# Performance work log

Measured on AMD Instinct MI355X. Metric: run time of the kernel, lower is better.

Reference implementation:

```python
import jax, jax.numpy as jnp
import numpy as np

DT = 0.01
T, B, I, H, O = 512, 128, 256, 1024, 256


def setup_inputs() -> dict:
    key = jax.random.key(0)
    ks = jax.random.split(key, 9)
    def xavier(k, out_f, in_f):
        lim = np.sqrt(6.0 / (in_f + out_f)).astype(np.float32)
        return jax.random.uniform(k, (out_f, in_f), jnp.float32, -lim, lim)
    return {
        "x": jax.random.normal(ks[0], (T, B, I), jnp.float32),
        "W_h": xavier(ks[1], H, I + H),                      # HRCell linear, no bias
        "gain": jnp.ones((H,), jnp.float32),
        "omega": jax.random.uniform(ks[2], (H,), jnp.float32, 10.0, 50.0),
        "b_offset": jax.random.uniform(ks[3], (H,), jnp.float32, 1.0, 6.0),
        "W_o": xavier(ks[4], H, H),                          # LICell linear, no bias
        "tau_mem": 20.0 + 5.0 * jax.random.normal(ks[5], (H,), jnp.float32),
        "W_out": xavier(ks[6], O, H),                        # readout Linear
        "b_out": jnp.zeros((O,), jnp.float32),
    }


def reference(x, W_h, gain, omega, b_offset, W_o, tau_mem, W_out, b_out):
    om = jnp.abs(omega)
    om2 = om * om
    b = om2 * 0.005 + jnp.abs(b_offset)          # damping coefficient per unit
    alpha = jnp.exp(-1.0 / jnp.abs(tau_mem))     # leaky-integrator decay
    Bsz = x.shape[1]
    Hd = W_h.shape[0]
    Od = W_out.shape[0]

    def step(carry, x_t):
        hu, hv, ou, acc = carry
        # HRCell: linear on concat(input, hidden_u), then harmonic update
        in_sum = jnp.concatenate([x_t, hu], axis=1) @ W_h.T   # [B, H]
        hv = hv + hu * DT
        hu = hu + in_sum * DT - b * hu * (2.0 * DT) - om2 * hv * DT
        hu = hu * gain                                        # normalize=False path
        # LICell: leaky integrator on projected hidden
        ou = ou * alpha + (hu @ W_o.T) * (1.0 - alpha)
        # readout, summed over time
        acc = acc + ou @ W_out.T + b_out
        return (hu, hv, ou, acc), None

    z = jnp.zeros((Bsz, Hd), x.dtype)
    init = (z, z, z, jnp.zeros((Bsz, Od), x.dtype))
    (hu, hv, ou, acc), _ = jax.lax.scan(step, init, x)
    return acc
```

## Files before the change

kernel.cpp:

```cpp
#include <hip/hip_runtime.h>
#include <math.h>

#define DT 0.01f
constexpr int T = 512, B = 128, I = 256, H = 1024, O = 256;
constexpr int K = I + H;

constexpr size_t OFF_OSUM  = 0;
constexpr size_t OFF_HUH0  = OFF_OSUM + (size_t)B * H;
constexpr size_t OFF_HUL0  = OFF_HUH0 + (size_t)B * H / 2;
constexpr size_t OFF_HUH1  = OFF_HUL0 + (size_t)B * H / 2;
constexpr size_t OFF_HUL1  = OFF_HUH1 + (size_t)B * H / 2;
constexpr size_t OFF_COEF  = OFF_HUL1 + (size_t)B * H / 2;
constexpr size_t OFF_FLAGS = OFF_COEF + 5 * (size_t)H;
constexpr size_t OFF_WHH   = OFF_FLAGS + 8192;
constexpr size_t OFF_WHL   = OFF_WHH + 64 * 40 * 64 * 8 / 2;
constexpr size_t OFF_WOH   = OFF_WHL + 64 * 40 * 64 * 8 / 2;
constexpr size_t OFF_WOL   = OFF_WOH + 64 * 32 * 64 * 8 / 2;

constexpr int SM_WHH  = 0;
constexpr int SM_WHL  = 65536;
constexpr int SM_REDS = 131072;
constexpr int SM_REDP = 139520;
constexpr int SM_BYTES = 147968;

typedef __attribute__((ext_vector_type(8))) short short8v;
typedef __attribute__((ext_vector_type(4))) float f32x4;

static __device__ inline short f2bf(float f) {
    unsigned u = __builtin_bit_cast(unsigned, f);
    u += 0x7fffu + ((u >> 16) & 1u);
    return (short)(u >> 16);
}
static __device__ inline float bf2f(short s) {
    return __builtin_bit_cast(float, ((unsigned)(unsigned short)s) << 16);
}

__global__ __launch_bounds__(256)
void init_kernel(float* __restrict__ ws, const float* __restrict__ omega,
                 const float* __restrict__ b_offset, const float* __restrict__ tau_mem,
                 const float* __restrict__ gain) {
    size_t tid = (size_t)blockIdx.x * blockDim.x + threadIdx.x;
    size_t stride = (size_t)gridDim.x * blockDim.x;
    for (size_t i = tid; i < (size_t)B * H; i += stride) ws[OFF_HUH0 + i] = 0.0f;
    for (size_t i = tid; i < 8192; i += stride) ws[OFF_FLAGS + i] = 0.0f;
    if (tid < H) {
        float om  = fabsf(omega[tid]);
        float om2 = om * om;
        float bb  = om2 * 0.005f + fabsf(b_offset[tid]);
        float al  = expf(-1.0f / fabsf(tau_mem[tid]));
        float g   = gain[tid];
        ws[OFF_COEF + 0 * H + tid] = g * (1.0f - 2.0f * bb * DT);
        ws[OFF_COEF + 1 * H + tid] = g * DT;
        ws[OFF_COEF + 2 * H + tid] = g * om2 * DT;
        ws[OFF_COEF + 3 * H + tid] = al;
        ws[OFF_COEF + 4 * H + tid] = 1.0f - al;
    }
}

template <int NKS, int KD>
__global__ __launch_bounds__(256)
void convert_kernel(const float* __restrict__ W, short* __restrict__ WH,
                    short* __restrict__ WL) {
    int g = blockIdx.x * 256 + threadIdx.x;
    int lane = g & 63;
    int ks = (g >> 6) % NKS;
    int cg = g / (NKS * 64);
    int col = cg * 16 + (lane & 15);
    int k = ks * 32 + ((lane >> 4) << 3);
    const float* src = W + (size_t)col * KD + k;
    short8v hi, lo;
    #pragma unroll
    for (int j = 0; j < 8; ++j) {
        float v = src[j];
        short h = f2bf(v);
        hi[j] = h;
        lo[j] = f2bf(v - bf2f(h));
    }
    *(short8v*)(WH + (size_t)g * 8) = hi;
    *(short8v*)(WL + (size_t)g * 8) = lo;
}

__global__ __launch_bounds__(512)
void rnn_persist(const float* __restrict__ x, float* __restrict__ ws) {
    extern __shared__ char sm[];
    float* redS = (float*)(sm + SM_REDS);
    float* redP = (float*)(sm + SM_REDP);
    __shared__ int role_sm;

    const float* coef = ws + OFF_COEF;
    float* osum_g = ws + OFF_OSUM;
    const short* huhS[2] = {(const short*)(ws + OFF_HUH0), (const short*)(ws + OFF_HUH1)};
    const short* hulS[2] = {(const short*)(ws + OFF_HUL0), (const short*)(ws + OFF_HUL1)};
    unsigned int* huhW[2] = {(unsigned int*)(ws + OFF_HUH0), (unsigned int*)(ws + OFF_HUH1)};
    unsigned int* hulW[2] = {(unsigned int*)(ws + OFF_HUL0), (unsigned int*)(ws + OFF_HUL1)};
    int* flags = (int*)(ws + OFF_FLAGS);
    int* ctr   = flags + 4096;

    const int tid = threadIdx.x;

    if (tid == 0) {
        unsigned xcc_;
        asm volatile("s_getreg_b32 %0, hwreg(HW_REG_XCC_ID)" : "=s"(xcc_));
        int slot = atomicAdd(ctr + (xcc_ & 7), 1);
        role_sm = (int)((xcc_ & 7) * 32 + (slot & 31));
    }
    __syncthreads();
    const int role = role_sm;
    const int xcc = role >> 5;
    const int g   = role & 31;
    const int col0 = g * 32, row0 = xcc * 16;

    const int wid = tid >> 6, lane = tid & 63;
    const int ntile = wid & 1, ksl = wid >> 1;
    const int colgrp = 2 * g + ntile;
    const int rowg = row0 + (lane & 15);
    const int koff = (lane >> 4) << 3;

    {
        const float4* srcH = (const float4*)(ws + OFF_WHH);
        const float4* srcL = (const float4*)(ws + OFF_WHL);
        float4* dH = (float4*)(sm + SM_WHH);
        float4* dL = (float4*)(sm + SM_WHL);
        for (int i = tid; i < 2 * 2048; i += 512) {
            int n = i >> 11, rem = i & 2047;
            dH[i] = srcH[((size_t)(2 * g + n) * 40 + 8) * 64 + rem];
            dL[i] = srcL[((size_t)(2 * g + n) * 40 + 8) * 64 + rem];
        }
    }
    short8v woh[8], wxh[2], wxl[2];
    {
        const short8v* WOHg = (const short8v*)(ws + OFF_WOH) + (size_t)colgrp * 32 * 64 + lane;
        const short8v* WXH  = (const short8v*)(ws + OFF_WHH) + (size_t)colgrp * 40 * 64 + lane;
        const short8v* WXL  = (const short8v*)(ws + OFF_WHL) + (size_t)colgrp * 40 * 64 + lane;
        #pragma unroll
        for (int j = 0; j < 8; ++j) woh[j] = WOHg[(ksl * 8 + j) * 64];
        #pragma unroll
        for (int j = 0; j < 2; ++j) { wxh[j] = WXH[(ksl * 2 + j) * 64]; wxl[j] = WXL[(ksl * 2 + j) * 64]; }
    }
    __syncthreads();

    const short8v* lWHH = (const short8v*)(sm + SM_WHH) + (size_t)ntile * 2048 + lane;
    const short8v* lWHL = (const short8v*)(sm + SM_WHL) + (size_t)ntile * 2048 + lane;

    const int er = tid >> 4;
    const int ec0 = (tid & 15) * 2;
    const int gcol0 = col0 + ec0;
    const size_t erow = (size_t)(row0 + (er & 15));
    float k1a=0,k1b=0,k2a=0,k2b=0,k3a=0,k3b=0, ala=0,alb=0,alma=0,almb=0;
    if (tid < 256) {
        k1a = coef[gcol0];         k1b = coef[gcol0 + 1];
        k2a = coef[H + gcol0];     k2b = coef[H + gcol0 + 1];
        k3a = coef[2 * H + gcol0]; k3b = coef[2 * H + gcol0 + 1];
        ala = coef[3 * H + gcol0]; alb = coef[3 * H + gcol0 + 1];
        alma = coef[4 * H + gcol0]; almb = coef[4 * H + gcol0 + 1];
    }
    float hva=0,hvb=0,oua=0,oub=0,osa=0,osb=0,hua=0,hub=0;

    int* myflag = flags + ((xcc * 32 + g) << 4);
    const size_t rowOffH = (size_t)rowg * H + koff;

    for (int s = 0; s <= T; ++s) {
        const bool last = (s == T);
        f32x4 accS = {0, 0, 0, 0}, accP = {0, 0, 0, 0};

        if (!last) {
            const float* xrow = x + (size_t)s * B * I + (size_t)rowg * I + koff;
            #pragma unroll
            for (int j = 0; j < 2; ++j) {
                float4 a0 = *(const float4*)(xrow + (ksl * 2 + j) * 32);
                float4 a1 = *(const float4*)(xrow + (ksl * 2 + j) * 32 + 4);
                float av[8] = {a0.x,a0.y,a0.z,a0.w,a1.x,a1.y,a1.z,a1.w};
                short8v ah, alv;
                #pragma unroll
                for (int q = 0; q < 8; ++q) {
                    short h = f2bf(av[q]);
                    ah[q] = h;
                    alv[q] = f2bf(av[q] - bf2f(h));
                }
                accS = __builtin_amdgcn_mfma_f32_16x16x32_bf16(ah, wxh[j], accS, 0,0,0);
                accS = __builtin_amdgcn_mfma_f32_16x16x32_bf16(alv, wxh[j], accS, 0,0,0);
                accS = __builtin_amdgcn_mfma_f32_16x16x32_bf16(ah, wxl[j], accS, 0,0,0);
            }
        }

        if (tid < 32) {
            int* pollp = flags + ((xcc * 32 + tid) << 4);
            while (__hip_atomic_load(pollp, __ATOMIC_RELAXED, __HIP_MEMORY_SCOPE_AGENT) < s)
                __builtin_amdgcn_s_sleep(1);
        }
        __syncthreads();
        asm volatile("" ::: "memory");

        const short* hb_ = huhS[s & 1] + rowOffH;
        const short* lb_ = hulS[s & 1] + rowOffH;
        short8v hbuf[8], lbuf[8];
        #pragma unroll
        for (int j = 0; j < 8; ++j) {
            asm volatile("global_load_dwordx4 %0, %1, off sc0" : "=v"(hbuf[j]) : "v"(hb_ + (ksl * 8 + j) * 32));
            asm volatile("global_load_dwordx4 %0, %1, off sc0" : "=v"(lbuf[j]) : "v"(lb_ + (ksl * 8 + j) * 32));
        }
        if (s > 0 && tid < 256) {
            const float* rp = redP + er * 33 + ec0;
            float p0 = (rp[0] + rp[528]) + (rp[1056] + rp[1584]);
            float p1 = (rp[1] + rp[529]) + (rp[1057] + rp[1585]);
            oua = oua * ala + p0 * alma; osa += oua;
            oub = oub * alb + p1 * almb; osb += oub;
        }

        if (!last) {
            asm volatile("s_waitcnt vmcnt(8)");
            __builtin_amdgcn_sched_barrier(0);
            #pragma unroll
            for (int j = 0; j < 4; ++j) {
                short8v ch = lWHH[(ksl * 8 + j) * 64];
                short8v cl = lWHL[(ksl * 8 + j) * 64];
                accS = __builtin_amdgcn_mfma_f32_16x16x32_bf16(hbuf[j], ch, accS, 0,0,0);
                accS = __builtin_amdgcn_mfma_f32_16x16x32_bf16(lbuf[j], ch, accS, 0,0,0);
                accS = __builtin_amdgcn_mfma_f32_16x16x32_bf16(hbuf[j], cl, accS, 0,0,0);
            }
            asm volatile("s_waitcnt vmcnt(0)");
            __builtin_amdgcn_sched_barrier(0);
            #pragma unroll
            for (int j = 4; j < 8; ++j) {
                short8v ch = lWHH[(ksl * 8 + j) * 64];
                short8v cl = lWHL[(ksl * 8 + j) * 64];
                accS = __builtin_amdgcn_mfma_f32_16x16x32_bf16(hbuf[j], ch, accS, 0,0,0);
                accS = __builtin_amdgcn_mfma_f32_16x16x32_bf16(lbuf[j], ch, accS, 0,0,0);
                accS = __builtin_amdgcn_mfma_f32_16x16x32_bf16(hbuf[j], cl, accS, 0,0,0);
            }
            #pragma unroll
            for (int r = 0; r < 4; ++r) {
                int crow = ((lane >> 4) << 2) + r;
                redS[ksl * 528 + crow * 33 + ntile * 16 + (lane & 15)] = accS[r];
            }
            __syncthreads();

            if (tid < 256) {
                const float* rs = redS + er * 33 + ec0;
                float s0 = (rs[0] + rs[528]) + (rs[1056] + rs[1584]);
                float s1 = (rs[1] + rs[529]) + (rs[1057] + rs[1585]);
                float hvn0 = hva + hua * DT;
                float hun0 = k1a * hua + k2a * s0 - k3a * hvn0;
                hva = hvn0; hua = hun0;
                float hvn1 = hvb + hub * DT;
                float hun1 = k1b * hub + k2b * s1 - k3b * hvn1;
                hvb = hvn1; hub = hun1;
                short h0 = f2bf(hun0), h1 = f2bf(hun1);
                short l0 = f2bf(hun0 - bf2f(h0)), l1 = f2bf(hun1 - bf2f(h1));
                unsigned hp = (unsigned)(unsigned short)h0 | ((unsigned)(unsigned short)h1 << 16);
                unsigned lp = (unsigned)(unsigned short)l0 | ((unsigned)(unsigned short)l1 << 16);
                size_t off32 = (erow * H + gcol0) >> 1;
                unsigned int* hp_ = huhW[(s + 1) & 1] + off32;
                unsigned int* lp_ = hulW[(s + 1) & 1] + off32;
                asm volatile("global_store_dword %0, %1, off sc0" :: "v"(hp_), "v"(hp) : "memory");
                asm volatile("global_store_dword %0, %1, off sc0" :: "v"(lp_), "v"(lp) : "memory");
            }
            asm volatile("s_waitcnt vmcnt(0)" ::: "memory");
            __syncthreads();
            if (tid == 0)
                __hip_atomic_store(myflag, s + 1, __ATOMIC_RELAXED, __HIP_MEMORY_SCOPE_AGENT);
        } else {
            asm volatile("s_waitcnt vmcnt(0)");
            __builtin_amdgcn_sched_barrier(0);
            __syncthreads();
        }

        #pragma unroll
        for (int j = 0; j < 8; ++j) {
            accP = __builtin_amdgcn_mfma_f32_16x16x32_bf16(hbuf[j], woh[j], accP, 0,0,0);
            accP = __builtin_amdgcn_mfma_f32_16x16x32_bf16(lbuf[j], woh[j], accP, 0,0,0);
        }
        #pragma unroll
        for (int r = 0; r < 4; ++r) {
            int crow = ((lane >> 4) << 2) + r;
            redP[ksl * 528 + crow * 33 + ntile * 16 + (lane & 15)] = accP[r];
        }
    }

    __syncthreads();
    if (tid < 256) {
        const float* rp = redP + er * 33 + ec0;
        float p0 = (rp[0] + rp[528]) + (rp[1056] + rp[1584]);
        float p1 = (rp[1] + rp[529]) + (rp[1057] + rp[1585]);
        float o0 = oua * ala + p0 * alma; osa += o0;
        float o1 = oub * alb + p1 * almb; osb += o1;
        osum_g[erow * H + gcol0] = osa;
        osum_g[erow * H + gcol0 + 1] = osb;
    }
}

__global__ __launch_bounds__(256)
void readout_kernel(const float* __restrict__ ou_sum, const float* __restrict__ W_out,
                    const float* __restrict__ b_out, float* __restrict__ out) {
    constexpr int KC = 128, BT = 32, CT = 16;
    __shared__ float act[BT][KC + 4];
    __shared__ float w[CT][KC + 4];
    int wg = blockIdx.x;
    int bt = wg & 3, cg = wg >> 2;
    int row0 = bt * BT, col0 = cg * CT;
    int tid = threadIdx.x;
    int c = tid & 15, rr = tid >> 4;

    float4 acc0 = {0, 0, 0, 0}, acc1 = {0, 0, 0, 0};
    for (int kc = 0; kc < H / KC; ++kc) {
        int k0 = kc * KC;
        for (int i = tid; i < BT * (KC / 4); i += 256) {
            int r = i >> 5, c4 = (i & 31) * 4;
            *(float4*)&act[r][c4] = *(const float4*)&ou_sum[(size_t)(row0 + r) * H + k0 + c4];
        }
        for (int i = tid; i < CT * (KC / 4); i += 256) {
            int r = i >> 5, c4 = (i & 31) * 4;
            *(float4*)&w[r][c4] = *(const float4*)&W_out[(size_t)(col0 + r) * H + k0 + c4];
        }
        __syncthreads();
        #pragma unroll
        for (int k4 = 0; k4 < KC / 4; ++k4) {
            float4 a0 = *(const float4*)&act[rr][k4 * 4];
            float4 a1 = *(const float4*)&act[rr + 16][k4 * 4];
            float4 w0 = *(const float4*)&w[c][k4 * 4];
            acc0.x = fmaf(a0.x, w0.x, acc0.x); acc0.y = fmaf(a0.y, w0.y, acc0.y);
            acc0.z = fmaf(a0.z, w0.z, acc0.z); acc0.w = fmaf(a0.w, w0.w, acc0.w);
            acc1.x = fmaf(a1.x, w0.x, acc1.x); acc1.y = fmaf(a1.y, w0.y, acc1.y);
            acc1.z = fmaf(a1.z, w0.z, acc1.z); acc1.w = fmaf(a1.w, w0.w, acc1.w);
        }
        __syncthreads();
    }
    float v0 = (acc0.x + acc0.y) + (acc0.z + acc0.w);
    float v1 = (acc1.x + acc1.y) + (acc1.z + acc1.w);
    int gcol = col0 + c;
    float bo = b_out[gcol] * (float)T;
    out[(size_t)(row0 + rr) * O + gcol] = v0 + bo;
    out[(size_t)(row0 + rr + 16) * O + gcol] = v1 + bo;
}

extern "C" void kernel_launch(void* const* d_in, const int* in_sizes, int n_in,
                              void* d_out, int out_size, void* d_ws, size_t ws_size,
                              hipStream_t stream) {
    const float* x        = (const float*)d_in[0];
    const float* W_h      = (const float*)d_in[1];
    const float* gain     = (const float*)d_in[2];
    const float* omega    = (const float*)d_in[3];
    const float* b_offset = (const float*)d_in[4];
    const float* W_o      = (const float*)d_in[5];
    const float* tau_mem  = (const float*)d_in[6];
    const float* W_out    = (const float*)d_in[7];
    const float* b_out    = (const float*)d_in[8];
    float* ws  = (float*)d_ws;
    float* out = (float*)d_out;

    init_kernel<<<512, 256, 0, stream>>>(ws, omega, b_offset, tau_mem, gain);
    convert_kernel<40, K><<<640, 256, 0, stream>>>(
        W_h, (short*)(ws + OFF_WHH), (short*)(ws + OFF_WHL));
    convert_kernel<32, H><<<512, 256, 0, stream>>>(
        W_o, (short*)(ws + OFF_WOH), (short*)(ws + OFF_WOL));

    rnn_persist<<<256, 512, SM_BYTES, stream>>>(x, ws);

    readout_kernel<<<64, 256, 0, stream>>>(ws + OFF_OSUM, W_out, b_out, out);
}
```

Measured before the change: 3.717 ms.

## Split MFMA accumulators and add fast sc0 flag polling with safe fallback

Each MFMA reduction chain now alternates between two accumulators, which shortens the dependency chain between back-to-back MFMAs. Inter-block step flags are duplicated: a fast copy is written and polled with sc0 plain loads/stores, and a safe copy uses agent-scope atomics and is checked every 64 spins. The aim is lower latency in the per-step cross-workgroup barrier of the persistent recurrent kernel. The fast flag path relies on cache coherence behaviour that is not guaranteed, so the atomic fallback is there to avoid hangs.

```diff
diff --git a/kernel.cpp b/kernel.cpp
--- a/kernel.cpp
+++ b/kernel.cpp
@@ -12,7 +12,7 @@
 constexpr size_t OFF_HUL1  = OFF_HUH1 + (size_t)B * H / 2;
 constexpr size_t OFF_COEF  = OFF_HUL1 + (size_t)B * H / 2;
 constexpr size_t OFF_FLAGS = OFF_COEF + 5 * (size_t)H;
-constexpr size_t OFF_WHH   = OFF_FLAGS + 8192;
+constexpr size_t OFF_WHH   = OFF_FLAGS + 8256;
 constexpr size_t OFF_WHL   = OFF_WHH + 64 * 40 * 64 * 8 / 2;
 constexpr size_t OFF_WOH   = OFF_WHL + 64 * 40 * 64 * 8 / 2;
 constexpr size_t OFF_WOL   = OFF_WOH + 64 * 32 * 64 * 8 / 2;
@@ -42,7 +42,7 @@
     size_t tid = (size_t)blockIdx.x * blockDim.x + threadIdx.x;
     size_t stride = (size_t)gridDim.x * blockDim.x;
     for (size_t i = tid; i < (size_t)B * H; i += stride) ws[OFF_HUH0 + i] = 0.0f;
-    for (size_t i = tid; i < 8192; i += stride) ws[OFF_FLAGS + i] = 0.0f;
+    for (size_t i = tid; i < 8256; i += stride) ws[OFF_FLAGS + i] = 0.0f;
     if (tid < H) {
         float om  = fabsf(omega[tid]);
         float om2 = om * om;
@@ -94,7 +94,7 @@
     unsigned int* huhW[2] = {(unsigned int*)(ws + OFF_HUH0), (unsigned int*)(ws + OFF_HUH1)};
     unsigned int* hulW[2] = {(unsigned int*)(ws + OFF_HUL0), (unsigned int*)(ws + OFF_HUL1)};
     int* flags = (int*)(ws + OFF_FLAGS);
-    int* ctr   = flags + 4096;
+    int* ctr   = flags + 8192;
 
     const int tid = threadIdx.x;
 
@@ -156,12 +156,16 @@
     }
     float hva=0,hvb=0,oua=0,oub=0,osa=0,osb=0,hua=0,hub=0;
 
-    int* myflag = flags + ((xcc * 32 + g) << 4);
+    int* myfast = flags + ((xcc * 32 + g) << 4);
+    int* mysafe = flags + 4096 + ((xcc * 32 + g) << 4);
+    const int* fastp = flags + ((xcc * 32 + (tid & 31)) << 4);
+    int* safep = flags + 4096 + ((xcc * 32 + (tid & 31)) << 4);
     const size_t rowOffH = (size_t)rowg * H + koff;
 
     for (int s = 0; s <= T; ++s) {
         const bool last = (s == T);
-        f32x4 accS = {0, 0, 0, 0}, accP = {0, 0, 0, 0};
+        f32x4 accS = {0,0,0,0}, accS2 = {0,0,0,0};
+        f32x4 accP = {0,0,0,0}, accP2 = {0,0,0,0};
 
         if (!last) {
             const float* xrow = x + (size_t)s * B * I + (size_t)rowg * I + koff;
@@ -177,16 +181,25 @@
                     ah[q] = h;
                     alv[q] = f2bf(av[q] - bf2f(h));
                 }
-                accS = __builtin_amdgcn_mfma_f32_16x16x32_bf16(ah, wxh[j], accS, 0,0,0);
-                accS = __builtin_amdgcn_mfma_f32_16x16x32_bf16(alv, wxh[j], accS, 0,0,0);
-                accS = __builtin_amdgcn_mfma_f32_16x16x32_bf16(ah, wxl[j], accS, 0,0,0);
+                f32x4* acc = j ? &accS2 : &accS;
+                *acc = __builtin_amdgcn_mfma_f32_16x16x32_bf16(ah, wxh[j], *acc, 0,0,0);
+                *acc = __builtin_amdgcn_mfma_f32_16x16x32_bf16(alv, wxh[j], *acc, 0,0,0);
+                *acc = __builtin_amdgcn_mfma_f32_16x16x32_bf16(ah, wxl[j], *acc, 0,0,0);
             }
         }
 
         if (tid < 32) {
-            int* pollp = flags + ((xcc * 32 + tid) << 4);
-            while (__hip_atomic_load(pollp, __ATOMIC_RELAXED, __HIP_MEMORY_SCOPE_AGENT) < s)
+            int v, spins = 0;
+            for (;;) {
+                asm volatile("global_load_dword %0, %1, off sc0\n\ts_waitcnt vmcnt(0)"
+                             : "=v"(v) : "v"(fastp) : "memory");
+                if (v >= s) break;
+                if ((++spins & 63) == 0) {
+                    v = __hip_atomic_load(safep, __ATOMIC_RELAXED, __HIP_MEMORY_SCOPE_AGENT);
+                    if (v >= s) break;
+                }
                 __builtin_amdgcn_s_sleep(1);
+            }
         }
         __syncthreads();
         asm volatile("" ::: "memory");
@@ -214,9 +227,10 @@
             for (int j = 0; j < 4; ++j) {
                 short8v ch = lWHH[(ksl * 8 + j) * 64];
                 short8v cl = lWHL[(ksl * 8 + j) * 64];
-                accS = __builtin_amdgcn_mfma_f32_16x16x32_bf16(hbuf[j], ch, accS, 0,0,0);
-                accS = __builtin_amdgcn_mfma_f32_16x16x32_bf16(lbuf[j], ch, accS, 0,0,0);
-                accS = __builtin_amdgcn_mfma_f32_16x16x32_bf16(hbuf[j], cl, accS, 0,0,0);
+                f32x4* acc = (j & 1) ? &accS2 : &accS;
+                *acc = __builtin_amdgcn_mfma_f32_16x16x32_bf16(hbuf[j], ch, *acc, 0,0,0);
+                *acc = __builtin_amdgcn_mfma_f32_16x16x32_bf16(lbuf[j], ch, *acc, 0,0,0);
+                *acc = __builtin_amdgcn_mfma_f32_16x16x32_bf16(hbuf[j], cl, *acc, 0,0,0);
             }
             asm volatile("s_waitcnt vmcnt(0)");
             __builtin_amdgcn_sched_barrier(0);
@@ -224,14 +238,15 @@
             for (int j = 4; j < 8; ++j) {
                 short8v ch = lWHH[(ksl * 8 + j) * 64];
                 short8v cl = lWHL[(ksl * 8 + j) * 64];
-                accS = __builtin_amdgcn_mfma_f32_16x16x32_bf16(hbuf[j], ch, accS, 0,0,0);
-                accS = __builtin_amdgcn_mfma_f32_16x16x32_bf16(lbuf[j], ch, accS, 0,0,0);
-                accS = __builtin_amdgcn_mfma_f32_16x16x32_bf16(hbuf[j], cl, accS, 0,0,0);
+                f32x4* acc = (j & 1) ? &accS2 : &accS;
+                *acc = __builtin_amdgcn_mfma_f32_16x16x32_bf16(hbuf[j], ch, *acc, 0,0,0);
+                *acc = __builtin_amdgcn_mfma_f32_16x16x32_bf16(lbuf[j], ch, *acc, 0,0,0);
+                *acc = __builtin_amdgcn_mfma_f32_16x16x32_bf16(hbuf[j], cl, *acc, 0,0,0);
             }
             #pragma unroll
             for (int r = 0; r < 4; ++r) {
                 int crow = ((lane >> 4) << 2) + r;
-                redS[ksl * 528 + crow * 33 + ntile * 16 + (lane & 15)] = accS[r];
+                redS[ksl * 528 + crow * 33 + ntile * 16 + (lane & 15)] = accS[r] + accS2[r];
             }
             __syncthreads();
 
@@ -257,8 +272,11 @@
             }
             asm volatile("s_waitcnt vmcnt(0)" ::: "memory");
             __syncthreads();
-            if (tid == 0)
-                __hip_atomic_store(myflag, s + 1, __ATOMIC_RELAXED, __HIP_MEMORY_SCOPE_AGENT);
+            if (tid == 0) {
+                int fv = s + 1;
+                asm volatile("global_store_dword %0, %1, off sc0" :: "v"(myfast), "v"(fv) : "memory");
+                __hip_atomic_store(mysafe, fv, __ATOMIC_RELAXED, __HIP_MEMORY_SCOPE_AGENT);
+            }
         } else {
             asm volatile("s_waitcnt vmcnt(0)");
             __builtin_amdgcn_sched_barrier(0);
@@ -267,13 +285,14 @@
 
         #pragma unroll
         for (int j = 0; j < 8; ++j) {
-            accP = __builtin_amdgcn_mfma_f32_16x16x32_bf16(hbuf[j], woh[j], accP, 0,0,0);
-            accP = __builtin_amdgcn_mfma_f32_16x16x32_bf16(lbuf[j], woh[j], accP, 0,0,0);
+            f32x4* acc = (j & 1) ? &accP2 : &accP;
+            *acc = __builtin_amdgcn_mfma_f32_16x16x32_bf16(hbuf[j], woh[j], *acc, 0,0,0);
+            *acc = __builtin_amdgcn_mfma_f32_16x16x32_bf16(lbuf[j], woh[j], *acc, 0,0,0);
         }
         #pragma unroll
         for (int r = 0; r < 4; ++r) {
             int crow = ((lane >> 4) << 2) + r;
-            redP[ksl * 528 + crow * 33 + ntile * 16 + (lane & 15)] = accP[r];
+            redP[ksl * 528 + crow * 33 + ntile * 16 + (lane & 15)] = accP[r] + accP2[r];
         }
     }
 
```

After: 3.790 ms. No clear change (+2.0%).

## Split persistent workgroups into recurrence and output-projection roles with reader flags

Applied to the files above, without the earlier changes.

The persistent RNN kernel now splits each XCC's 32 workgroups into two roles. Sixteen compute the hidden recurrence over 64-column tiles. The other sixteen compute the W_o projection and leaky integration from the published hidden state, one step behind. Recurrence workgroups now wait on both writer and reader flags before overwriting the double buffer. The goal is to take the W_o matmul off the serial critical path of the recurrence. The cost is that each recurrence workgroup does twice the K-columns, streams W_h low-part weights from global memory every step, and carries extra cross-workgroup synchronization.

```diff
diff --git a/kernel.cpp b/kernel.cpp
--- a/kernel.cpp
+++ b/kernel.cpp
@@ -12,16 +12,13 @@
 constexpr size_t OFF_HUL1  = OFF_HUH1 + (size_t)B * H / 2;
 constexpr size_t OFF_COEF  = OFF_HUL1 + (size_t)B * H / 2;
 constexpr size_t OFF_FLAGS = OFF_COEF + 5 * (size_t)H;
-constexpr size_t OFF_WHH   = OFF_FLAGS + 8192;
+constexpr size_t OFF_WHH   = OFF_FLAGS + 8224;
 constexpr size_t OFF_WHL   = OFF_WHH + 64 * 40 * 64 * 8 / 2;
 constexpr size_t OFF_WOH   = OFF_WHL + 64 * 40 * 64 * 8 / 2;
 constexpr size_t OFF_WOL   = OFF_WOH + 64 * 32 * 64 * 8 / 2;
 
-constexpr int SM_WHH  = 0;
-constexpr int SM_WHL  = 65536;
-constexpr int SM_REDS = 131072;
-constexpr int SM_REDP = 139520;
-constexpr int SM_BYTES = 147968;
+constexpr int SM_RED   = 131072;
+constexpr int SM_BYTES = 131072 + 2 * 16 * 68 * 4;
 
 typedef __attribute__((ext_vector_type(8))) short short8v;
 typedef __attribute__((ext_vector_type(4))) float f32x4;
@@ -42,7 +39,7 @@
     size_t tid = (size_t)blockIdx.x * blockDim.x + threadIdx.x;
     size_t stride = (size_t)gridDim.x * blockDim.x;
     for (size_t i = tid; i < (size_t)B * H; i += stride) ws[OFF_HUH0 + i] = 0.0f;
-    for (size_t i = tid; i < 8192; i += stride) ws[OFF_FLAGS + i] = 0.0f;
+    for (size_t i = tid; i < 8224; i += stride) ws[OFF_FLAGS + i] = 0.0f;
     if (tid < H) {
         float om  = fabsf(omega[tid]);
         float om2 = om * om;
@@ -83,18 +80,17 @@
 __global__ __launch_bounds__(512)
 void rnn_persist(const float* __restrict__ x, float* __restrict__ ws) {
     extern __shared__ char sm[];
-    float* redS = (float*)(sm + SM_REDS);
-    float* redP = (float*)(sm + SM_REDP);
+    float* red = (float*)(sm + SM_RED);
     __shared__ int role_sm;
 
     const float* coef = ws + OFF_COEF;
     float* osum_g = ws + OFF_OSUM;
     const short* huhS[2] = {(const short*)(ws + OFF_HUH0), (const short*)(ws + OFF_HUH1)};
     const short* hulS[2] = {(const short*)(ws + OFF_HUL0), (const short*)(ws + OFF_HUL1)};
-    unsigned int* huhW[2] = {(unsigned int*)(ws + OFF_HUH0), (unsigned int*)(ws + OFF_HUH1)};
-    unsigned int* hulW[2] = {(unsigned int*)(ws + OFF_HUL0), (unsigned int*)(ws + OFF_HUL1)};
+    short* huhW[2] = {(short*)(ws + OFF_HUH0), (short*)(ws + OFF_HUH1)};
+    short* hulW[2] = {(short*)(ws + OFF_HUL0), (short*)(ws + OFF_HUL1)};
     int* flags = (int*)(ws + OFF_FLAGS);
-    int* ctr   = flags + 4096;
+    int* ctr   = flags + 8192;
 
     const int tid = threadIdx.x;
 
@@ -106,186 +102,244 @@
     }
     __syncthreads();
     const int role = role_sm;
-    const int xcc = role >> 5;
-    const int g   = role & 31;
-    const int col0 = g * 32, row0 = xcc * 16;
+    const int xcc  = role >> 5;
+    const int slot = role & 31;
+    const bool isZ = (slot < 16);
+    const int g    = slot & 15;
+    const int row0 = xcc * 16;
 
     const int wid = tid >> 6, lane = tid & 63;
-    const int ntile = wid & 1, ksl = wid >> 1;
-    const int colgrp = 2 * g + ntile;
+    const int cgl = wid & 3, ksl = wid >> 2;
+    const int cg16 = 4 * g + cgl;
     const int rowg = row0 + (lane & 15);
     const int koff = (lane >> 4) << 3;
-
-    {
-        const float4* srcH = (const float4*)(ws + OFF_WHH);
-        const float4* srcL = (const float4*)(ws + OFF_WHL);
-        float4* dH = (float4*)(sm + SM_WHH);
-        float4* dL = (float4*)(sm + SM_WHL);
-        for (int i = tid; i < 2 * 2048; i += 512) {
-            int n = i >> 11, rem = i & 2047;
-            dH[i] = srcH[((size_t)(2 * g + n) * 40 + 8) * 64 + rem];
-            dL[i] = srcL[((size_t)(2 * g + n) * 40 + 8) * 64 + rem];
-        }
-    }
-    short8v woh[8], wxh[2], wxl[2];
-    {
-        const short8v* WOHg = (const short8v*)(ws + OFF_WOH) + (size_t)colgrp * 32 * 64 + lane;
-        const short8v* WXH  = (const short8v*)(ws + OFF_WHH) + (size_t)colgrp * 40 * 64 + lane;
-        const short8v* WXL  = (const short8v*)(ws + OFF_WHL) + (size_t)colgrp * 40 * 64 + lane;
-        #pragma unroll
-        for (int j = 0; j < 8; ++j) woh[j] = WOHg[(ksl * 8 + j) * 64];
-        #pragma unroll
-        for (int j = 0; j < 2; ++j) { wxh[j] = WXH[(ksl * 2 + j) * 64]; wxl[j] = WXL[(ksl * 2 + j) * 64]; }
-    }
-    __syncthreads();
-
-    const short8v* lWHH = (const short8v*)(sm + SM_WHH) + (size_t)ntile * 2048 + lane;
-    const short8v* lWHL = (const short8v*)(sm + SM_WHL) + (size_t)ntile * 2048 + lane;
+    const size_t rowOff = (size_t)rowg * H + koff;
+
+    int* flagbase = flags + xcc * 1024;
+    int* mywrite  = flagbase + g * 16;
+    int* myread   = flagbase + (16 + slot) * 16;
 
     const int er = tid >> 4;
-    const int ec0 = (tid & 15) * 2;
-    const int gcol0 = col0 + ec0;
+    const int c0 = (tid & 15) * 4;
+    const int gcol0 = g * 64 + c0;
     const size_t erow = (size_t)(row0 + (er & 15));
-    float k1a=0,k1b=0,k2a=0,k2b=0,k3a=0,k3b=0, ala=0,alb=0,alma=0,almb=0;
-    if (tid < 256) {
-        k1a = coef[gcol0];         k1b = coef[gcol0 + 1];
-        k2a = coef[H + gcol0];     k2b = coef[H + gcol0 + 1];
-        k3a = coef[2 * H + gcol0]; k3b = coef[2 * H + gcol0 + 1];
-        ala = coef[3 * H + gcol0]; alb = coef[3 * H + gcol0 + 1];
-        alma = coef[4 * H + gcol0]; almb = coef[4 * H + gcol0 + 1];
-    }
-    float hva=0,hvb=0,oua=0,oub=0,osa=0,osb=0,hua=0,hub=0;
-
-    int* myflag = flags + ((xcc * 32 + g) << 4);
-    const size_t rowOffH = (size_t)rowg * H + koff;
-
-    for (int s = 0; s <= T; ++s) {
-        const bool last = (s == T);
-        f32x4 accS = {0, 0, 0, 0}, accP = {0, 0, 0, 0};
-
-        if (!last) {
-            const float* xrow = x + (size_t)s * B * I + (size_t)rowg * I + koff;
-            #pragma unroll
-            for (int j = 0; j < 2; ++j) {
-                float4 a0 = *(const float4*)(xrow + (ksl * 2 + j) * 32);
-                float4 a1 = *(const float4*)(xrow + (ksl * 2 + j) * 32 + 4);
-                float av[8] = {a0.x,a0.y,a0.z,a0.w,a1.x,a1.y,a1.z,a1.w};
-                short8v ah, alv;
-                #pragma unroll
-                for (int q = 0; q < 8; ++q) {
-                    short h = f2bf(av[q]);
-                    ah[q] = h;
-                    alv[q] = f2bf(av[q] - bf2f(h));
-                }
-                accS = __builtin_amdgcn_mfma_f32_16x16x32_bf16(ah, wxh[j], accS, 0,0,0);
-                accS = __builtin_amdgcn_mfma_f32_16x16x32_bf16(alv, wxh[j], accS, 0,0,0);
-                accS = __builtin_amdgcn_mfma_f32_16x16x32_bf16(ah, wxl[j], accS, 0,0,0);
-            }
-        }
-
-        if (tid < 32) {
-            int* pollp = flags + ((xcc * 32 + tid) << 4);
-            while (__hip_atomic_load(pollp, __ATOMIC_RELAXED, __HIP_MEMORY_SCOPE_AGENT) < s)
-                __builtin_amdgcn_s_sleep(1);
+
+    if (isZ) {
+        {
+            const float4* srcH = (const float4*)(ws + OFF_WHH);
+            float4* dH = (float4*)sm;
+            for (int i = tid; i < 4 * 2048; i += 512) {
+                int cc = i >> 11, rem = i & 2047;
+                dH[i] = srcH[((size_t)(4 * g + cc) * 40 + 8) * 64 + rem];
+            }
+        }
+        short8v wxh[4], wxl[4];
+        {
+            const short8v* WXH = (const short8v*)(ws + OFF_WHH) + (size_t)cg16 * 40 * 64 + lane;
+            const short8v* WXL = (const short8v*)(ws + OFF_WHL) + (size_t)cg16 * 40 * 64 + lane;
+            #pragma unroll
+            for (int j = 0; j < 4; ++j) { wxh[j] = WXH[(ksl * 4 + j) * 64]; wxl[j] = WXL[(ksl * 4 + j) * 64]; }
         }
         __syncthreads();
-        asm volatile("" ::: "memory");
-
-        const short* hb_ = huhS[s & 1] + rowOffH;
-        const short* lb_ = hulS[s & 1] + rowOffH;
-        short8v hbuf[8], lbuf[8];
-        #pragma unroll
-        for (int j = 0; j < 8; ++j) {
-            asm volatile("global_load_dwordx4 %0, %1, off sc0" : "=v"(hbuf[j]) : "v"(hb_ + (ksl * 8 + j) * 32));
-            asm volatile("global_load_dwordx4 %0, %1, off sc0" : "=v"(lbuf[j]) : "v"(lb_ + (ksl * 8 + j) * 32));
-        }
-        if (s > 0 && tid < 256) {
-            const float* rp = redP + er * 33 + ec0;
-            float p0 = (rp[0] + rp[528]) + (rp[1056] + rp[1584]);
-            float p1 = (rp[1] + rp[529]) + (rp[1057] + rp[1585]);
-            oua = oua * ala + p0 * alma; osa += oua;
-            oub = oub * alb + p1 * almb; osb += oub;
-        }
-
-        if (!last) {
-            asm volatile("s_waitcnt vmcnt(8)");
-            __builtin_amdgcn_sched_barrier(0);
-            #pragma unroll
-            for (int j = 0; j < 4; ++j) {
-                short8v ch = lWHH[(ksl * 8 + j) * 64];
-                short8v cl = lWHL[(ksl * 8 + j) * 64];
-                accS = __builtin_amdgcn_mfma_f32_16x16x32_bf16(hbuf[j], ch, accS, 0,0,0);
-                accS = __builtin_amdgcn_mfma_f32_16x16x32_bf16(lbuf[j], ch, accS, 0,0,0);
-                accS = __builtin_amdgcn_mfma_f32_16x16x32_bf16(hbuf[j], cl, accS, 0,0,0);
-            }
-            asm volatile("s_waitcnt vmcnt(0)");
-            __builtin_amdgcn_sched_barrier(0);
-            #pragma unroll
-            for (int j = 4; j < 8; ++j) {
-                short8v ch = lWHH[(ksl * 8 + j) * 64];
-                short8v cl = lWHL[(ksl * 8 + j) * 64];
-                accS = __builtin_amdgcn_mfma_f32_16x16x32_bf16(hbuf[j], ch, accS, 0,0,0);
-                accS = __builtin_amdgcn_mfma_f32_16x16x32_bf16(lbuf[j], ch, accS, 0,0,0);
-                accS = __builtin_amdgcn_mfma_f32_16x16x32_bf16(hbuf[j], cl, accS, 0,0,0);
+        const short8v* lWHH = (const short8v*)sm + (size_t)cgl * 2048 + lane;
+        const short8v* WHLg = (const short8v*)(ws + OFF_WHL) + ((size_t)cg16 * 40 + 8) * 64 + lane;
+
+        float k1[4], k2[4], k3[4];
+        float hu4[4] = {0,0,0,0}, hv4[4] = {0,0,0,0};
+        if (tid < 256) {
+            #pragma unroll
+            for (int c = 0; c < 4; ++c) {
+                k1[c] = coef[gcol0 + c];
+                k2[c] = coef[H + gcol0 + c];
+                k3[c] = coef[2 * H + gcol0 + c];
+            }
+        }
+
+        for (int s = 0; s < T; ++s) {
+            f32x4 a1 = {0,0,0,0}, a2 = {0,0,0,0}, a3 = {0,0,0,0};
+
+            short8v whl[16];
+            #pragma unroll
+            for (int j = 0; j < 16; ++j) whl[j] = WHLg[(ksl * 16 + j) * 64];
+            {
+                const float* xrow = x + (size_t)s * B * I + (size_t)rowg * I + koff;
+                #pragma unroll
+                for (int j = 0; j < 4; ++j) {
+                    float4 q0 = *(const float4*)(xrow + (ksl * 4 + j) * 32);
+                    float4 q1 = *(const float4*)(xrow + (ksl * 4 + j) * 32 + 4);
+                    float av[8] = {q0.x,q0.y,q0.z,q0.w,q1.x,q1.y,q1.z,q1.w};
+                    short8v ah, alv;
+                    #pragma unroll
+                    for (int q = 0; q < 8; ++q) {
+                        short h = f2bf(av[q]);
+                        ah[q] = h;
+                        alv[q] = f2bf(av[q] - bf2f(h));
+                    }
+                    a1 = __builtin_amdgcn_mfma_f32_16x16x32_bf16(ah,  wxh[j], a1, 0,0,0);
+                    a2 = __builtin_amdgcn_mfma_f32_16x16x32_bf16(alv, wxh[j], a2, 0,0,0);
+                    a3 = __builtin_amdgcn_mfma_f32_16x16x32_bf16(ah,  wxl[j], a3, 0,0,0);
+                }
+            }
+
+            if (tid < 48) {
+                int* pollp = flagbase + tid * 16;
+                while (__hip_atomic_load(pollp, __ATOMIC_RELAXED, __HIP_MEMORY_SCOPE_AGENT) < s)
+                    __builtin_amdgcn_s_sleep(1);
+            }
+            __syncthreads();
+            asm volatile("" ::: "memory");
+
+            const short* hb = huhS[s & 1] + rowOff;
+            const short* lb = hulS[s & 1] + rowOff;
+            #pragma unroll
+            for (int b = 0; b < 2; ++b) {
+                short8v hbuf[8], lbuf[8];
+                #pragma unroll
+                for (int j = 0; j < 8; ++j) {
+                    asm volatile("global_load_dwordx4 %0, %1, off sc0" : "=v"(hbuf[j]) : "v"(hb + (ksl * 16 + b * 8 + j) * 32));
+                    asm volatile("global_load_dwordx4 %0, %1, off sc0" : "=v"(lbuf[j]) : "v"(lb + (ksl * 16 + b * 8 + j) * 32));
+                }
+                asm volatile("s_waitcnt vmcnt(8)");
+                __builtin_amdgcn_sched_barrier(0);
+                #pragma unroll
+                for (int j = 0; j < 4; ++j) {
+                    short8v ch = lWHH[(ksl * 16 + b * 8 + j) * 64];
+                    a1 = __builtin_amdgcn_mfma_f32_16x16x32_bf16(hbuf[j], ch, a1, 0,0,0);
+                    a2 = __builtin_amdgcn_mfma_f32_16x16x32_bf16(lbuf[j], ch, a2, 0,0,0);
+                    a3 = __builtin_amdgcn_mfma_f32_16x16x32_bf16(hbuf[j], whl[b * 8 + j], a3, 0,0,0);
+                }
+                asm volatile("s_waitcnt vmcnt(0)");
+                __builtin_amdgcn_sched_barrier(0);
+                #pragma unroll
+                for (int j = 4; j < 8; ++j) {
+                    short8v ch = lWHH[(ksl * 16 + b * 8 + j) * 64];
+                    a1 = __builtin_amdgcn_mfma_f32_16x16x32_bf16(hbuf[j], ch, a1, 0,0,0);
+                    a2 = __builtin_amdgcn_mfma_f32_16x16x32_bf16(lbuf[j], ch, a2, 0,0,0);
+                    a3 = __builtin_amdgcn_mfma_f32_16x16x32_bf16(hbuf[j], whl[b * 8 + j], a3, 0,0,0);
+                }
             }
             #pragma unroll
             for (int r = 0; r < 4; ++r) {
                 int crow = ((lane >> 4) << 2) + r;
-                redS[ksl * 528 + crow * 33 + ntile * 16 + (lane & 15)] = accS[r];
-            }
-            __syncthreads();
+                red[ksl * 1088 + crow * 68 + cgl * 16 + (lane & 15)] = (a1[r] + a2[r]) + a3[r];
+            }
+            __syncthreads();
+            if (tid == 0)
+                __hip_atomic_store(myread, s + 1, __ATOMIC_RELAXED, __HIP_MEMORY_SCOPE_AGENT);
 
             if (tid < 256) {
-                const float* rs = redS + er * 33 + ec0;
-                float s0 = (rs[0] + rs[528]) + (rs[1056] + rs[1584]);
-                float s1 = (rs[1] + rs[529]) + (rs[1057] + rs[1585]);
-                float hvn0 = hva + hua * DT;
-                float hun0 = k1a * hua + k2a * s0 - k3a * hvn0;
-                hva = hvn0; hua = hun0;
-                float hvn1 = hvb + hub * DT;
-                float hun1 = k1b * hub + k2b * s1 - k3b * hvn1;
-                hvb = hvn1; hub = hun1;
-                short h0 = f2bf(hun0), h1 = f2bf(hun1);
-                short l0 = f2bf(hun0 - bf2f(h0)), l1 = f2bf(hun1 - bf2f(h1));
-                unsigned hp = (unsigned)(unsigned short)h0 | ((unsigned)(unsigned short)h1 << 16);
-                unsigned lp = (unsigned)(unsigned short)l0 | ((unsigned)(unsigned short)l1 << 16);
-                size_t off32 = (erow * H + gcol0) >> 1;
-                unsigned int* hp_ = huhW[(s + 1) & 1] + off32;
-                unsigned int* lp_ = hulW[(s + 1) & 1] + off32;
-                asm volatile("global_store_dword %0, %1, off sc0" :: "v"(hp_), "v"(hp) : "memory");
-                asm volatile("global_store_dword %0, %1, off sc0" :: "v"(lp_), "v"(lp) : "memory");
+                short hh[4], ll[4];
+                #pragma unroll
+                for (int c = 0; c < 4; ++c) {
+                    float si = red[er * 68 + c0 + c] + red[1088 + er * 68 + c0 + c];
+                    float hvn = hv4[c] + hu4[c] * DT;
+                    float hun = k1[c] * hu4[c] + k2[c] * si - k3[c] * hvn;
+                    hv4[c] = hvn;
+                    hu4[c] = hun;
+                    hh[c] = f2bf(hun);
+                    ll[c] = f2bf(hun - bf2f(hh[c]));
+                }
+                unsigned long long hp = (unsigned long long)(unsigned short)hh[0]
+                    | ((unsigned long long)(unsigned short)hh[1] << 16)
+                    | ((unsigned long long)(unsigned short)hh[2] << 32)
+                    | ((unsigned long long)(unsigned short)hh[3] << 48);
+                unsigned long long lp = (unsigned long long)(unsigned short)ll[0]
+                    | ((unsigned long long)(unsigned short)ll[1] << 16)
+                    | ((unsigned long long)(unsigned short)ll[2] << 32)
+                    | ((unsigned long long)(unsigned short)ll[3] << 48);
+                short* hdst = huhW[(s + 1) & 1] + erow * H + gcol0;
+                short* ldst = hulW[(s + 1) & 1] + erow * H + gcol0;
+                asm volatile("global_store_dwordx2 %0, %1, off sc0" :: "v"(hdst), "v"(hp) : "memory");
+                asm volatile("global_store_dwordx2 %0, %1, off sc0" :: "v"(ldst), "v"(lp) : "memory");
             }
             asm volatile("s_waitcnt vmcnt(0)" ::: "memory");
             __syncthreads();
             if (tid == 0)
-                __hip_atomic_store(myflag, s + 1, __ATOMIC_RELAXED, __HIP_MEMORY_SCOPE_AGENT);
-        } else {
-            asm volatile("s_waitcnt vmcnt(0)");
-            __builtin_amdgcn_sched_barrier(0);
-            __syncthreads();
-        }
-
-        #pragma unroll
-        for (int j = 0; j < 8; ++j) {
-            accP = __builtin_amdgcn_mfma_f32_16x16x32_bf16(hbuf[j], woh[j], accP, 0,0,0);
-            accP = __builtin_amdgcn_mfma_f32_16x16x32_bf16(lbuf[j], woh[j], accP, 0,0,0);
-        }
-        #pragma unroll
-        for (int r = 0; r < 4; ++r) {
-            int crow = ((lane >> 4) << 2) + r;
-            redP[ksl * 528 + crow * 33 + ntile * 16 + (lane & 15)] = accP[r];
-        }
-    }
-
-    __syncthreads();
-    if (tid < 256) {
-        const float* rp = redP + er * 33 + ec0;
-        float p0 = (rp[0] + rp[528]) + (rp[1056] + rp[1584]);
-        float p1 = (rp[1] + rp[529]) + (rp[1057] + rp[1585]);
-        float o0 = oua * ala + p0 * alma; osa += o0;
-        float o1 = oub * alb + p1 * almb; osb += o1;
-        osum_g[erow * H + gcol0] = osa;
-        osum_g[erow * H + gcol0 + 1] = osb;
+                __hip_atomic_store(mywrite, s + 1, __ATOMIC_RELAXED, __HIP_MEMORY_SCOPE_AGENT);
+        }
+    } else {
+        {
+            const float4* srcO = (const float4*)(ws + OFF_WOH);
+            float4* dO = (float4*)sm;
+            for (int i = tid; i < 4 * 2048; i += 512) {
+                int cc = i >> 11, rem = i & 2047;
+                dO[i] = srcO[(size_t)(4 * g + cc) * 32 * 64 + rem];
+            }
+        }
+        __syncthreads();
+        const short8v* lWOH = (const short8v*)sm + (size_t)cgl * 2048 + lane;
+
+        float al4[4], alm4[4];
+        float ou4[4] = {0,0,0,0}, os4[4] = {0,0,0,0};
+        if (tid < 256) {
+            #pragma unroll
+            for (int c = 0; c < 4; ++c) {
+                al4[c]  = coef[3 * H + gcol0 + c];
+                alm4[c] = coef[4 * H + gcol0 + c];
+            }
+        }
+
+        for (int s = 0; s <= T; ++s) {
+            if (tid < 16) {
+                int* pollp = flagbase + tid * 16;
+                while (__hip_atomic_load(pollp, __ATOMIC_RELAXED, __HIP_MEMORY_SCOPE_AGENT) < s)
+                    __builtin_amdgcn_s_sleep(1);
+            }
+            __syncthreads();
+            asm volatile("" ::: "memory");
+
+            const short* hb = huhS[s & 1] + rowOff;
+            const short* lb = hulS[s & 1] + rowOff;
+            f32x4 p1 = {0,0,0,0}, p2 = {0,0,0,0};
+            #pragma unroll
+            for (int b = 0; b < 2; ++b) {
+                short8v hbuf[8], lbuf[8];
+                #pragma unroll
+                for (int j = 0; j < 8; ++j) {
+                    asm volatile("global_load_dwordx4 %0, %1, off sc0" : "=v"(hbuf[j]) : "v"(hb + (ksl * 16 + b * 8 + j) * 32));
+                    asm volatile("global_load_dwordx4 %0, %1, off sc0" : "=v"(lbuf[j]) : "v"(lb + (ksl * 16 + b * 8 + j) * 32));
+                }
+                asm volatile("s_waitcnt vmcnt(8)");
+                __builtin_amdgcn_sched_barrier(0);
+                #pragma unroll
+                for (int j = 0; j < 4; ++j) {
+                    short8v wo = lWOH[(ksl * 16 + b * 8 + j) * 64];
+                    p1 = __builtin_amdgcn_mfma_f32_16x16x32_bf16(hbuf[j], wo, p1, 0,0,0);
+                    p2 = __builtin_amdgcn_mfma_f32_16x16x32_bf16(lbuf[j], wo, p2, 0,0,0);
+                }
+                asm volatile("s_waitcnt vmcnt(0)");
+                __builtin_amdgcn_sched_barrier(0);
+                #pragma unroll
+                for (int j = 4; j < 8; ++j) {
+                    short8v wo = lWOH[(ksl * 16 + b * 8 + j) * 64];
+                    p1 = __builtin_amdgcn_mfma_f32_16x16x32_bf16(hbuf[j], wo, p1, 0,0,0);
+                    p2 = __builtin_amdgcn_mfma_f32_16x16x32_bf16(lbuf[j], wo, p2, 0,0,0);
+                }
+            }
+            #pragma unroll
+            for (int r = 0; r < 4; ++r) {
+                int crow = ((lane >> 4) << 2) + r;
+                red[ksl * 1088 + crow * 68 + cgl * 16 + (lane & 15)] = p1[r] + p2[r];
+            }
+            __syncthreads();
+            if (tid == 0)
+                __hip_atomic_store(myread, s + 1, __ATOMIC_RELAXED, __HIP_MEMORY_SCOPE_AGENT);
+
+            if (tid < 256) {
+                #pragma unroll
+                for (int c = 0; c < 4; ++c) {
+                    float q = red[er * 68 + c0 + c] + red[1088 + er * 68 + c0 + c];
+                    ou4[c] = al4[c] * ou4[c] + alm4[c] * q;
+                    os4[c] += ou4[c];
+                }
+            }
+            __syncthreads();
+        }
+        if (tid < 256) {
+            #pragma unroll
+            for (int c = 0; c < 4; ++c)
+                osum_g[erow * H + gcol0 + c] = os4[c];
+        }
     }
 }
 
```

Result: slower. 6.457 ms (+73.7%).
